# Kernel optimization log

Hardware: AMD Instinct MI355X
Metric: run time of the kernel (lower is better)

## Reference

```python
import jax, jax.numpy as jnp
import numpy as np
from jax import lax

# Grid / layer constants matching init_kwargs
D, H, W = 41, 159, 159   # spatial_shape (chosen so (dim-K) % S == 0)
K = 3                    # kernel_size
S = 2                    # stride
CIN, COUT = 32, 64       # in_channels, out_channels
B = 2                    # batch_size
N_PER_BATCH = 75000      # active voxels per batch element (unique coords)


def setup_inputs() -> dict:
    # Unique active-voxel coordinates per batch (spconv assumes no duplicates).
    rng = np.random.default_rng(0)
    nvox = D * H * W
    rows = []
    for b in range(B):
        lin = rng.choice(nvox, size=N_PER_BATCH, replace=False)
        z = lin // (H * W)
        y = (lin // W) % H
        x = lin % W
        rows.append(np.stack([np.full(N_PER_BATCH, b), z, y, x], axis=1))
    coors = jnp.asarray(np.concatenate(rows, axis=0), dtype=jnp.int32)  # [N,4]

    key = jax.random.key(0)
    k1, k2, k3 = jax.random.split(key, 3)
    features = jax.random.normal(k1, (B * N_PER_BATCH, CIN), dtype=jnp.float32)
    # SparseConv3d weight (no bias): kernel [K,K,K,CIN,COUT] in DHWIO layout.
    w1 = (jax.random.normal(k2, (K, K, K, CIN, COUT), dtype=jnp.float32) * 0.05)
    # SparseInverseConv3d weight: transpose-conv mapping COUT -> CIN; stored in
    # forward-conv DHWIO layout [K,K,K,CIN,COUT] and applied via conv_transpose
    # with transpose_kernel=True (the exact adjoint of the forward conv op).
    w2 = (jax.random.normal(k3, (K, K, K, CIN, COUT), dtype=jnp.float32) * 0.05)
    return {"features": features, "coors": coors, "batch_size": B, "w1": w1, "w2": w2}


def reference(features, coors, batch_size, w1, w2):
    # Scatter active features into a dense NDHWC grid (equivalent to the sparse
    # tensor; SparseConv3d with bias=False gives identical values on active sites).
    b, z, y, x = coors[:, 0], coors[:, 1], coors[:, 2], coors[:, 3]
    dense = jnp.zeros((batch_size, D, H, W, CIN), features.dtype).at[b, z, y, x].set(features)
    # Mask of originally-active sites: SparseInverseConv3d (shared indice_key)
    # only produces outputs at these sites, and ToDense zeros everything else.
    mask = jnp.zeros((batch_size, D, H, W, 1), features.dtype).at[b, z, y, x].set(1.0)

    dn = ("NDHWC", "DHWIO", "NDHWC")
    # SparseConv3d(CIN->COUT, k=3, s=2): strided VALID conv.
    mid = lax.conv_general_dilated(dense, w1, (S, S, S), "VALID", dimension_numbers=dn)
    # SparseInverseConv3d(COUT->CIN): exact transpose of the forward conv's
    # gather/scatter pattern; recovers the original spatial shape.
    back = lax.conv_transpose(mid, w2, (S, S, S), "VALID", dimension_numbers=dn,
                              transpose_kernel=True)
    out = back * mask  # restrict to original active sites, zeros elsewhere
    return jnp.transpose(out, (0, 4, 1, 2, 3))  # ToDense returns NCDHW
```

## Files before the change

kernel.cpp:

```cpp
#include <hip/hip_runtime.h>

#define D_   41
#define H_   159
#define W_   159
#define MD   20
#define MH   79
#define MW   79
#define CIN  32
#define COUT 64
#define BATCH 2

#define NTAP 27
#define WLDS (NTAP * 16 * 64)

#define BLK   1024
#define WPB   (BLK / 64)

typedef unsigned int u32;
typedef unsigned short u16;
typedef _Float16 f16;
typedef f16 f16x2 __attribute__((ext_vector_type(2)));

static __device__ __forceinline__ u32 f16pair(float a, float b) {
    f16x2 h = { (f16)a, (f16)b };
    return __builtin_bit_cast(u32, h);
}
static __device__ __forceinline__ float dot2(u32 a, u32 b, float c) {
    return __builtin_amdgcn_fdot2(__builtin_bit_cast(f16x2, a),
                                  __builtin_bit_cast(f16x2, b), c, false);
}

__global__ void pack_kernel(const float* __restrict__ w1, const float* __restrict__ w2,
                            u32* __restrict__ w1p, u32* __restrict__ w2p) {
    int i = blockIdx.x * 256 + threadIdx.x;
    if (i >= WLDS) return;
    int k  = i & 3;
    int co = (i >> 2) & 63;
    int j4 = (i >> 8) & 3;
    int t  = i >> 10;
    int j  = j4 * 4 + k;
    int s0 = (t * 32 + 2 * j) * 64 + co;
    int s1 = (t * 32 + 2 * j + 1) * 64 + co;
    w1p[i] = f16pair(w1[s0], w1[s1]);
    w2p[i] = f16pair(w2[s0], w2[s1]);
}

__global__ void featpack_kernel(const float* __restrict__ feat,
                                u32* __restrict__ feat_h, int n16) {
    int i = blockIdx.x * 256 + threadIdx.x;
    if (i >= n16) return;
    int p = i >> 4, j = i & 15;
    feat_h[i] = f16pair(feat[p * CIN + 2 * j], feat[p * CIN + 2 * j + 1]);
}

__global__ void scatter_idx_kernel(const int* __restrict__ coors,
                                   int* __restrict__ idx, int n) {
    int i = blockIdx.x * blockDim.x + threadIdx.x;
    if (i >= n) return;
    int4 c = ((const int4*)coors)[i];
    idx[((c.x * D_ + c.y) * H_ + c.z) * W_ + c.w] = i;
}

#define LOADW(dst, base, t)                                        \
    {                                                              \
        const uint4* wq = (const uint4*)(base) + (t) * 256 + lane; \
        uint4 q0 = wq[0], q1 = wq[64], q2 = wq[128], q3 = wq[192]; \
        dst[0] = q0.x;  dst[1] = q0.y;  dst[2] = q0.z;  dst[3] = q0.w;   \
        dst[4] = q1.x;  dst[5] = q1.y;  dst[6] = q1.z;  dst[7] = q1.w;   \
        dst[8] = q2.x;  dst[9] = q2.y;  dst[10] = q2.z; dst[11] = q2.w;  \
        dst[12] = q3.x; dst[13] = q3.y; dst[14] = q3.z; dst[15] = q3.w;  \
    }

__global__ __launch_bounds__(BLK) void mid_kernel(const u32* __restrict__ feat_h,
                                                  const int* __restrict__ idx,
                                                  const u32* __restrict__ w1p,
                                                  u16* __restrict__ mid_h) {
    __shared__ u32 lw[WLDS];
    for (int i = threadIdx.x; i < WLDS; i += BLK) lw[i] = w1p[i];
    __syncthreads();

    const int NV = BATCH * MD * MH * MW;
    int lane = threadIdx.x & 63;
    int wid  = threadIdx.x >> 6;
    int nw   = gridDim.x * WPB;
    int gw   = blockIdx.x * WPB + wid;
    int per  = (NV + nw - 1) / nw;
    int v0   = gw * per;
    int v1   = v0 + per; if (v1 > NV) v1 = NV;

    int l  = lane < NTAP ? lane : NTAP - 1;
    int kz = l / 9, kr = l % 9, ky = kr / 3, kx = kr % 3;

    auto probe = [&](int v) -> int {
        if (v >= v1 || lane >= NTAP) return -1;
        int xo = v % MW; int t0 = v / MW;
        int yo = t0 % MH; t0 /= MH;
        int zo = t0 % MD; int b = t0 / MD;
        return idx[((b * D_ + 2 * zo + kz) * H_ + 2 * yo + ky) * W_ + 2 * xo + kx];
    };

    int pA = probe(v0), pB = probe(v0 + 1);
    for (int v = v0; v < v1; v += 2) {
        int cA = pA, cB = pB;
        pA = probe(v + 2);
        pB = probe(v + 3);
        unsigned long long mA = __ballot(cA >= 0);
        unsigned long long mB = __ballot(cB >= 0);

        float a0 = 0.f, a1 = 0.f, b0 = 0.f, b1 = 0.f;
        while (mA | mB) {
            bool hA = mA != 0, hB = mB != 0;
            uint4 fa0, fa1, fa2, fa3, fb0, fb1, fb2, fb3;
            u32 wav[16], wbv[16];
            if (hA) {
                int t = (int)__builtin_ctzll(mA); mA &= mA - 1;
                int pp = __shfl(cA, t);
                const uint4* f4 = (const uint4*)(feat_h + (size_t)pp * 16);
                fa0 = f4[0]; fa1 = f4[1]; fa2 = f4[2]; fa3 = f4[3];
                LOADW(wav, lw, t)
            }
            if (hB) {
                int t = (int)__builtin_ctzll(mB); mB &= mB - 1;
                int pp = __shfl(cB, t);
                const uint4* f4 = (const uint4*)(feat_h + (size_t)pp * 16);
                fb0 = f4[0]; fb1 = f4[1]; fb2 = f4[2]; fb3 = f4[3];
                LOADW(wbv, lw, t)
            }
            if (hA) {
                a0 = dot2(fa0.x, wav[0],  a0);  a1 = dot2(fa0.y, wav[1],  a1);
                a0 = dot2(fa0.z, wav[2],  a0);  a1 = dot2(fa0.w, wav[3],  a1);
                a0 = dot2(fa1.x, wav[4],  a0);  a1 = dot2(fa1.y, wav[5],  a1);
                a0 = dot2(fa1.z, wav[6],  a0);  a1 = dot2(fa1.w, wav[7],  a1);
                a0 = dot2(fa2.x, wav[8],  a0);  a1 = dot2(fa2.y, wav[9],  a1);
                a0 = dot2(fa2.z, wav[10], a0);  a1 = dot2(fa2.w, wav[11], a1);
                a0 = dot2(fa3.x, wav[12], a0);  a1 = dot2(fa3.y, wav[13], a1);
                a0 = dot2(fa3.z, wav[14], a0);  a1 = dot2(fa3.w, wav[15], a1);
            }
            if (hB) {
                b0 = dot2(fb0.x, wbv[0],  b0);  b1 = dot2(fb0.y, wbv[1],  b1);
                b0 = dot2(fb0.z, wbv[2],  b0);  b1 = dot2(fb0.w, wbv[3],  b1);
                b0 = dot2(fb1.x, wbv[4],  b0);  b1 = dot2(fb1.y, wbv[5],  b1);
                b0 = dot2(fb1.z, wbv[6],  b0);  b1 = dot2(fb1.w, wbv[7],  b1);
                b0 = dot2(fb2.x, wbv[8],  b0);  b1 = dot2(fb2.y, wbv[9],  b1);
                b0 = dot2(fb2.z, wbv[10], b0);  b1 = dot2(fb2.w, wbv[11], b1);
                b0 = dot2(fb3.x, wbv[12], b0);  b1 = dot2(fb3.y, wbv[13], b1);
                b0 = dot2(fb3.z, wbv[14], b0);  b1 = dot2(fb3.w, wbv[15], b1);
            }
        }
        {
            f16 hv = (f16)(a0 + a1);
            mid_h[(size_t)v * COUT + lane] = __builtin_bit_cast(u16, hv);
        }
        if (v + 1 < v1) {
            f16 hv = (f16)(b0 + b1);
            mid_h[(size_t)(v + 1) * COUT + lane] = __builtin_bit_cast(u16, hv);
        }
    }
}

#define BSTEP(MK, HALF)                                            \
    {                                                              \
        bool up = (lane & MK) != 0;                                \
        _Pragma("unroll")                                          \
        for (int k = 0; k < HALF; ++k) {                           \
            float send = up ? acc[k] : acc[k + HALF];              \
            float keep = up ? acc[k + HALF] : acc[k];              \
            acc[k] = keep + __shfl_xor(send, MK, 64);              \
        }                                                          \
    }

__global__ __launch_bounds__(BLK) void out_kernel(const int* __restrict__ coors,
                                                  const u16* __restrict__ mid_h,
                                                  const u32* __restrict__ w2p,
                                                  float* __restrict__ compact, int n) {
    __shared__ u32 lw[WLDS];
    for (int i = threadIdx.x; i < WLDS; i += BLK) lw[i] = w2p[i];
    __syncthreads();

    int lane = threadIdx.x & 63;
    int wid  = threadIdx.x >> 6;
    int nw   = gridDim.x * WPB;
    int gw   = blockIdx.x * WPB + wid;
    int per  = (n + nw - 1) / nw;
    int i0   = gw * per;
    int i1   = i0 + per; if (i1 > n) i1 = n;

    int l  = lane < NTAP ? lane : NTAP - 1;
    int kz = l / 9, kr = l % 9, ky = kr / 3, kx = kr % 3;

    const int4* cvec = (const int4*)coors;
    int4 nc = make_int4(0, 0, 0, 0);
    if (i0 < i1) nc = cvec[i0];

    for (int i = i0; i < i1; ++i) {
        int4 c = nc;
        if (i + 1 < i1) nc = cvec[i + 1];
        int b = c.x, z = c.y, y = c.z, x = c.w;

        int zr = z - kz, yr = y - ky, xr = x - kx;
        bool ok = (lane < NTAP) &&
                  zr >= 0 && !(zr & 1) && (zr >> 1) < MD &&
                  yr >= 0 && !(yr & 1) && (yr >> 1) < MH &&
                  xr >= 0 && !(xr & 1) && (xr >> 1) < MW;
        int vv = ok ? ((b * MD + (zr >> 1)) * MH + (yr >> 1)) * MW + (xr >> 1) : -1;
        unsigned long long m = __ballot(ok);

        float acc[CIN];
        #pragma unroll
        for (int ci = 0; ci < CIN; ++ci) acc[ci] = 0.f;

        while (m) {
            int t0 = (int)__builtin_ctzll(m); m &= m - 1;
            bool h1 = (m != 0);
            int t1 = 0;
            if (h1) { t1 = (int)__builtin_ctzll(m); m &= m - 1; }

            int ve0 = __shfl(vv, t0);
            u32 mr0 = mid_h[(size_t)ve0 * COUT + lane];
            u32 mr1 = 0;
            if (h1) {
                int ve1 = __shfl(vv, t1);
                mr1 = mid_h[(size_t)ve1 * COUT + lane];
            }
            u32 mrp = mr0 | (mr1 << 16);

            u32 wv0[16], wv1[16];
            LOADW(wv0, lw, t0)
            LOADW(wv1, lw, t1)

            #pragma unroll
            for (int j = 0; j < 16; ++j) {
                u32 wlo = __builtin_amdgcn_perm(wv1[j], wv0[j], 0x05040100u);
                u32 whi = __builtin_amdgcn_perm(wv1[j], wv0[j], 0x07060302u);
                acc[2 * j + 0] = dot2(mrp, wlo, acc[2 * j + 0]);
                acc[2 * j + 1] = dot2(mrp, whi, acc[2 * j + 1]);
            }
        }

        BSTEP(32, 16)
        BSTEP(16, 8)
        BSTEP(8, 4)
        BSTEP(4, 2)
        BSTEP(2, 1)
        float s = acc[0] + __shfl_xor(acc[0], 1, 64);
        if (!(lane & 1))
            compact[(size_t)i * CIN + (lane >> 1)] = s;
    }
}

__global__ __launch_bounds__(256) void expand_kernel(const int* __restrict__ idx,
                                                     const float* __restrict__ compact,
                                                     float* __restrict__ out) {
    const int HW    = H_ * W_;
    const int PLANE = D_ * HW;
    const int NVOX  = BATCH * PLANE;
    int g = blockIdx.x * 256 + threadIdx.x;
    if (g >= NVOX) return;

    int p   = idx[g];
    int b   = g / PLANE;
    int rem = g - b * PLANE;

    float r[CIN];
    if (p >= 0) {
        const float4* row = (const float4*)(compact + (size_t)p * CIN);
        #pragma unroll
        for (int q = 0; q < 8; ++q) {
            float4 v = row[q];
            r[4 * q + 0] = v.x; r[4 * q + 1] = v.y;
            r[4 * q + 2] = v.z; r[4 * q + 3] = v.w;
        }
    } else {
        #pragma unroll
        for (int q = 0; q < CIN; ++q) r[q] = 0.f;
    }

    float* o = out + (size_t)b * ((size_t)CIN * PLANE) + rem;
    #pragma unroll
    for (int ci = 0; ci < CIN; ++ci)
        __builtin_nontemporal_store(r[ci], o + (size_t)ci * PLANE);
}

extern "C" void kernel_launch(void* const* d_in, const int* in_sizes, int n_in,
                              void* d_out, int out_size, void* d_ws, size_t ws_size,
                              hipStream_t stream) {
    const float* feat  = (const float*)d_in[0];
    const int*   coors = (const int*)d_in[1];
    const float* w1    = (const float*)d_in[3];
    const float* w2    = (const float*)d_in[4];
    float*       out   = (float*)d_out;

    int n = in_sizes[0] / CIN;

    int*   idx      = (int*)d_ws;
    size_t idxBytes = (size_t)BATCH * D_ * H_ * W_ * sizeof(int);
    size_t midOff   = (idxBytes + 255) & ~(size_t)255;
    u16*   mid_h    = (u16*)((char*)d_ws + midOff);
    size_t wOff     = midOff + (size_t)BATCH * MD * MH * MW * COUT * sizeof(u16);
    wOff            = (wOff + 255) & ~(size_t)255;
    u32*   w1p      = (u32*)((char*)d_ws + wOff);
    u32*   w2p      = w1p + WLDS;
    float* compact  = (float*)(w2p + WLDS);
    u32*   feat_h   = (u32*)(compact + (size_t)n * CIN);

    (void)hipMemsetAsync(idx, 0xFF, idxBytes, stream);

    pack_kernel<<<(WLDS + 255) / 256, 256, 0, stream>>>(w1, w2, w1p, w2p);
    featpack_kernel<<<(n * 16 + 255) / 256, 256, 0, stream>>>(feat, feat_h, n * 16);
    scatter_idx_kernel<<<(n + 255) / 256, 256, 0, stream>>>(coors, idx, n);

    mid_kernel<<<256, BLK, 0, stream>>>(feat_h, idx, w1p, mid_h);
    out_kernel<<<256, BLK, 0, stream>>>(coors, mid_h, w2p, compact, n);

    const int NVOX = BATCH * D_ * H_ * W_;
    expand_kernel<<<(NVOX + 255) / 256, 256, 0, stream>>>(idx, compact, out);
}
```

Before: 561.2 us.

## Sort active voxels spatially via count/scan/place and remap out_kernel block order

```diff
diff --git a/kernel.cpp b/kernel.cpp
--- a/kernel.cpp
+++ b/kernel.cpp
@@ -15,6 +15,9 @@
 
 #define BLK   1024
 #define WPB   (BLK / 64)
+
+#define SGRID 256
+#define SBLK  256
 
 typedef unsigned int u32;
 typedef unsigned short u16;
@@ -61,6 +64,59 @@
     idx[((c.x * D_ + c.y) * H_ + c.z) * W_ + c.w] = i;
 }
 
+
+__global__ __launch_bounds__(SBLK) void count_kernel(const int* __restrict__ idx,
+                                                     int* __restrict__ counts) {
+    const int NG = BATCH * D_ * H_ * W_;
+    int per = (NG + SGRID - 1) / SGRID;
+    int g0 = blockIdx.x * per;
+    int g1 = g0 + per; if (g1 > NG) g1 = NG;
+    int c = 0;
+    for (int g = g0 + threadIdx.x; g < g1; g += SBLK) c += (idx[g] >= 0);
+    __shared__ int sc[SBLK];
+    sc[threadIdx.x] = c;
+    __syncthreads();
+    for (int s = SBLK / 2; s > 0; s >>= 1) {
+        if (threadIdx.x < s) sc[threadIdx.x] += sc[threadIdx.x + s];
+        __syncthreads();
+    }
+    if (threadIdx.x == 0) counts[blockIdx.x] = sc[0];
+}
+
+__global__ __launch_bounds__(SGRID) void prefix_kernel(int* __restrict__ counts,
+                                                       int* __restrict__ bases) {
+    __shared__ int tmp[SGRID];
+    int t = threadIdx.x;
+    tmp[t] = counts[t];
+    __syncthreads();
+    for (int off = 1; off < SGRID; off <<= 1) {
+        int u = (t >= off) ? tmp[t - off] : 0;
+        __syncthreads();
+        tmp[t] += u;
+        __syncthreads();
+    }
+    bases[t] = (t == 0) ? 0 : tmp[t - 1];
+}
+
+__global__ __launch_bounds__(SBLK) void place_kernel(const int* __restrict__ idx,
+                                                     const int* __restrict__ bases,
+                                                     int* __restrict__ rank,
+                                                     int* __restrict__ perm) {
+    const int NG = BATCH * D_ * H_ * W_;
+    int per = (NG + SGRID - 1) / SGRID;
+    int g0 = blockIdx.x * per;
+    int g1 = g0 + per; if (g1 > NG) g1 = NG;
+    __shared__ int ctr;
+    if (threadIdx.x == 0) ctr = bases[blockIdx.x];
+    __syncthreads();
+    for (int g = g0 + threadIdx.x; g < g1; g += SBLK) {
+        int p = idx[g];
+        int r = -1;
+        if (p >= 0) { r = atomicAdd(&ctr, 1); perm[r] = p; }
+        rank[g] = r;
+    }
+}
+
 #define LOADW(dst, base, t)                                        \
     {                                                              \
         const uint4* wq = (const uint4*)(base) + (t) * 256 + lane; \
@@ -170,17 +226,20 @@
     }
 
 __global__ __launch_bounds__(BLK) void out_kernel(const int* __restrict__ coors,
+                                                  const int* __restrict__ perm,
                                                   const u16* __restrict__ mid_h,
                                                   const u32* __restrict__ w2p,
-                                                  float* __restrict__ compact, int n) {
+                                                  float* __restrict__ compact2, int n) {
     __shared__ u32 lw[WLDS];
     for (int i = threadIdx.x; i < WLDS; i += BLK) lw[i] = w2p[i];
     __syncthreads();
+
+    int sb = (blockIdx.x & 7) * 32 + (blockIdx.x >> 3);
 
     int lane = threadIdx.x & 63;
     int wid  = threadIdx.x >> 6;
     int nw   = gridDim.x * WPB;
-    int gw   = blockIdx.x * WPB + wid;
+    int gw   = sb * WPB + wid;
     int per  = (n + nw - 1) / nw;
     int i0   = gw * per;
     int i1   = i0 + per; if (i1 > n) i1 = n;
@@ -189,13 +248,20 @@
     int kz = l / 9, kr = l % 9, ky = kr / 3, kx = kr % 3;
 
     const int4* cvec = (const int4*)coors;
+    int p1 = 0, p2 = 0;
     int4 nc = make_int4(0, 0, 0, 0);
-    if (i0 < i1) nc = cvec[i0];
+    if (i0 < i1)     { p1 = perm[i0]; nc = cvec[p1]; }
+    if (i0 + 1 < i1) { p2 = perm[i0 + 1]; }
 
     for (int i = i0; i < i1; ++i) {
         int4 c = nc;
-        if (i + 1 < i1) nc = cvec[i + 1];
+        int pw = p1;
+        p1 = p2;
+        if (i + 1 < i1) nc = cvec[p1];
+        if (i + 2 < i1) p2 = perm[i + 2];
+
         int b = c.x, z = c.y, y = c.z, x = c.w;
+        (void)pw;
 
         int zr = z - kz, yr = y - ky, xr = x - kx;
         bool ok = (lane < NTAP) &&
@@ -244,12 +310,12 @@
         BSTEP(2, 1)
         float s = acc[0] + __shfl_xor(acc[0], 1, 64);
         if (!(lane & 1))
-            compact[(size_t)i * CIN + (lane >> 1)] = s;
-    }
-}
-
-__global__ __launch_bounds__(256) void expand_kernel(const int* __restrict__ idx,
-                                                     const float* __restrict__ compact,
+            compact2[(size_t)i * CIN + (lane >> 1)] = s;
+    }
+}
+
+__global__ __launch_bounds__(256) void expand_kernel(const int* __restrict__ rank,
+                                                     const float* __restrict__ compact2,
                                                      float* __restrict__ out) {
     const int HW    = H_ * W_;
     const int PLANE = D_ * HW;
@@ -257,13 +323,13 @@
     int g = blockIdx.x * 256 + threadIdx.x;
     if (g >= NVOX) return;
 
-    int p   = idx[g];
+    int r0  = rank[g];
     int b   = g / PLANE;
     int rem = g - b * PLANE;
 
     float r[CIN];
-    if (p >= 0) {
-        const float4* row = (const float4*)(compact + (size_t)p * CIN);
+    if (r0 >= 0) {
+        const float4* row = (const float4*)(compact2 + (size_t)r0 * CIN);
         #pragma unroll
         for (int q = 0; q < 8; ++q) {
             float4 v = row[q];
@@ -300,8 +366,12 @@
     wOff            = (wOff + 255) & ~(size_t)255;
     u32*   w1p      = (u32*)((char*)d_ws + wOff);
     u32*   w2p      = w1p + WLDS;
-    float* compact  = (float*)(w2p + WLDS);
-    u32*   feat_h   = (u32*)(compact + (size_t)n * CIN);
+    float* compact2 = (float*)(w2p + WLDS);
+    u32*   feat_h   = (u32*)(compact2 + (size_t)n * CIN);
+    int*   rank     = (int*)(feat_h + (size_t)n * 16);
+    int*   perm     = rank + (size_t)BATCH * D_ * H_ * W_;
+    int*   counts   = perm + n;
+    int*   bases    = counts + SGRID;
 
     (void)hipMemsetAsync(idx, 0xFF, idxBytes, stream);
 
@@ -309,9 +379,13 @@
     featpack_kernel<<<(n * 16 + 255) / 256, 256, 0, stream>>>(feat, feat_h, n * 16);
     scatter_idx_kernel<<<(n + 255) / 256, 256, 0, stream>>>(coors, idx, n);
 
+    count_kernel<<<SGRID, SBLK, 0, stream>>>(idx, counts);
+    prefix_kernel<<<1, SGRID, 0, stream>>>(counts, bases);
+    place_kernel<<<SGRID, SBLK, 0, stream>>>(idx, bases, rank, perm);
+
     mid_kernel<<<256, BLK, 0, stream>>>(feat_h, idx, w1p, mid_h);
-    out_kernel<<<256, BLK, 0, stream>>>(coors, mid_h, w2p, compact, n);
+    out_kernel<<<256, BLK, 0, stream>>>(coors, perm, mid_h, w2p, compact2, n);
 
     const int NVOX = BATCH * D_ * H_ * W_;
-    expand_kernel<<<(NVOX + 255) / 256, 256, 0, stream>>>(idx, compact, out);
-}
+    expand_kernel<<<(NVOX + 255) / 256, 256, 0, stream>>>(rank, compact2, out);
+}
```

Result: slower. 600.9 us (+7.1%).
